# Kernel tuning notes

Hardware: AMD Instinct MI355X
Metric: run time of the kernel (lower is better)

Reference implementation:

```python
import jax, jax.numpy as jnp
import numpy as np

NLAYERS, NHEAD, ATTN_LEN, DMODEL, DHID, NTOKEN = 9, 2, 5, 128, 512, 2
HD = DMODEL // NHEAD
B, T, F = 4, 4096, 128
INV_SQRT_HD = 1.0 / float(np.sqrt(HD))


def setup_inputs() -> dict:
    key = jax.random.key(0)
    ks = iter(jax.random.split(key, 64))
    def w(shape, s=0.02):
        return jax.random.normal(next(ks), shape, jnp.float32) * s
    return dict(
        x=jax.random.normal(next(ks), (B, T, F), jnp.float32),
        conv1_w=w((32, 1, 5, 3)), conv1_b=jnp.zeros((32,), jnp.float32),
        conv2_w=w((64, 32, 1, 12)), conv2_b=jnp.zeros((64,), jnp.float32),
        conv3_w=w((DMODEL, 64, 3, 6)), conv3_b=jnp.zeros((DMODEL,), jnp.float32),
        ln1_s=jnp.ones((NLAYERS, DMODEL), jnp.float32), ln1_b=jnp.zeros((NLAYERS, DMODEL), jnp.float32),
        ln2_s=jnp.ones((NLAYERS, DMODEL), jnp.float32), ln2_b=jnp.zeros((NLAYERS, DMODEL), jnp.float32),
        Wq=w((NLAYERS, DMODEL, DMODEL)), bq=jnp.zeros((NLAYERS, DMODEL), jnp.float32),
        Wk=w((NLAYERS, DMODEL, DMODEL)), bk=jnp.zeros((NLAYERS, DMODEL), jnp.float32),
        Wv=w((NLAYERS, DMODEL, DMODEL)), bv=jnp.zeros((NLAYERS, DMODEL), jnp.float32),
        Wo=w((NLAYERS, DMODEL, DMODEL)), bo=jnp.zeros((NLAYERS, DMODEL), jnp.float32),
        Er=w((NLAYERS, NHEAD, ATTN_LEN, HD)),
        W1=w((NLAYERS, DMODEL, DHID)), b1=jnp.zeros((NLAYERS, DHID), jnp.float32),
        W2=w((NLAYERS, DHID, DMODEL)), b2=jnp.zeros((NLAYERS, DMODEL), jnp.float32),
        Wout=w((DMODEL, NTOKEN)), bout=jnp.zeros((NTOKEN,), jnp.float32),
        Wt=w((DMODEL, 300)), bt=jnp.zeros((300,), jnp.float32),
    )


def _ln(x, s, b, eps=1e-5):
    m = x.mean(-1, keepdims=True)
    v = ((x - m) ** 2).mean(-1, keepdims=True)
    return (x - m) * jax.lax.rsqrt(v + eps) * s + b


def _conv(x, w, b, pad_h):
    y = jax.lax.conv_general_dilated(x, w, (1, 1), ((pad_h, pad_h), (0, 0)),
                                     dimension_numbers=('NCHW', 'OIHW', 'NCHW'))
    return y + b[None, :, None, None]


def _pool3(x):
    # MaxPool2d(kernel=(1,3), stride=(1,3)) on freq axis
    return jax.lax.reduce_window(x, -jnp.inf, jax.lax.max, (1, 1, 1, 3), (1, 1, 1, 3), 'VALID')


def _attn(x, Wq, bq, Wk, bk, Wv, bv, Wo, bo, Er, layer):
    # Dilated windowed attention: query t attends to t + (k - attn_len//2)*2^layer
    Bb, Tt, D = x.shape
    dil = 2 ** layer
    c = ATTN_LEN // 2
    q = (x @ Wq + bq).reshape(Bb, Tt, NHEAD, HD)
    k = (x @ Wk + bk).reshape(Bb, Tt, NHEAD, HD)
    v = (x @ Wv + bv).reshape(Bb, Tt, NHEAD, HD)
    offs = (jnp.arange(Tt)[:, None] + (jnp.arange(ATTN_LEN) - c)[None, :] * dil)  # (T, a)
    valid = (offs >= 0) & (offs < Tt)
    idx = jnp.clip(offs, 0, Tt - 1)
    kg = k[:, idx]  # (B, T, a, H, hd)
    vg = v[:, idx]
    scores = (jnp.einsum('bthd,btahd->bhta', q, kg)
              + jnp.einsum('bthd,had->bhta', q, Er)) * INV_SQRT_HD
    scores = jnp.where(valid[None, None], scores, -jnp.inf)
    a = jax.nn.softmax(scores, axis=-1)
    out = jnp.einsum('bhta,btahd->bthd', a, vg).reshape(Bb, Tt, D)
    return out @ Wo + bo


def _forward(x, conv1_w, conv1_b, conv2_w, conv2_b, conv3_w, conv3_b,
             ln1_s, ln1_b, ln2_s, ln2_b, Wq, bq, Wk, bk, Wv, bv, Wo, bo, Er,
             W1, b1, W2, b2, Wout, bout, Wt, bt):
    h = x[:, None]                                    # (B,1,T,F)
    h = jax.nn.relu(_pool3(_conv(h, conv1_w, conv1_b, 2)))
    h = jax.nn.relu(_pool3(_conv(h, conv2_w, conv2_b, 0)))
    h = jax.nn.relu(_pool3(_conv(h, conv3_w, conv3_b, 1)))  # (B,D,T,1)
    h = h[:, :, :, 0].transpose(0, 2, 1)              # (B,T,D)
    skips = []
    for l in range(NLAYERS):
        skip = _attn(_ln(h, ln1_s[l], ln1_b[l]), Wq[l], bq[l], Wk[l], bk[l],
                     Wv[l], bv[l], Wo[l], bo[l], Er[l], l)
        h = h + skip
        z = _ln(h, ln2_s[l], ln2_b[l])
        h = h + jax.nn.relu(z @ W1[l] + b1[l]) @ W2[l] + b2[l]
        skips.append(skip)
    out = jax.nn.relu(h) @ Wout + bout                # (B,T,ntoken)
    t = jax.nn.relu(sum(skips)).mean(axis=1) @ Wt + bt  # (B,300)
    return out, t


def reference(x, conv1_w, conv1_b, conv2_w, conv2_b, conv3_w, conv3_b,
              ln1_s, ln1_b, ln2_s, ln2_b, Wq, bq, Wk, bk, Wv, bv, Wo, bo, Er,
              W1, b1, W2, b2, Wout, bout, Wt, bt):
    return _forward(x, conv1_w, conv1_b, conv2_w, conv2_b, conv3_w, conv3_b,
                    ln1_s, ln1_b, ln2_s, ln2_b, Wq, bq, Wk, bk, Wv, bv, Wo, bo, Er,
                    W1, b1, W2, b2, Wout, bout, Wt, bt)
```

## Files before the change

### kernel.cpp

```cpp
#include <hip/hip_runtime.h>

#define T_ 4096
#define B_ 4

typedef unsigned short u16;
typedef __bf16 bf16x8 __attribute__((ext_vector_type(8)));
typedef float f32x4 __attribute__((ext_vector_type(4)));

__device__ inline void splitbf(float v, u16& h, u16& l) {
  __bf16 hb = (__bf16)v;
  float r = v - (float)hb;
  __bf16 lb = (__bf16)r;
  h = __builtin_bit_cast(u16, hb);
  l = __builtin_bit_cast(u16, lb);
}

#define MFMA(a,b,c) __builtin_amdgcn_mfma_f32_16x16x32_bf16((a),(b),(c),0,0,0)

__global__ __launch_bounds__(256) void k_conv12m(
    const float* __restrict__ x, const float* __restrict__ w1,
    const float* __restrict__ b1,
    const u16* __restrict__ wh, const u16* __restrict__ wl,
    const float* __restrict__ b2,
    u16* __restrict__ oh, u16* __restrict__ ol)
{
  __shared__ float sx[12][130];
  __shared__ float w1s[480];
  __shared__ float b1s[32];
  __shared__ u16 sh[8*43*40];
  __shared__ u16 sl[8*43*40];
  __shared__ float dmp[4][15][66];
  const int tid = threadIdx.x;
  const int t0 = blockIdx.x * 8;
  const int b = blockIdx.y;
  const float* xb = x + (size_t)b*T_*128;
  for (int i = tid; i < 1536; i += 256) {
    int r = i >> 7, c = i & 127;
    int t = t0 - 2 + r;
    sx[r][c] = (t >= 0 && t < T_) ? xb[t*128 + c] : 0.f;
  }
  for (int i = tid; i < 480; i += 256) w1s[i] = w1[i];
  if (tid < 32) b1s[tid] = b1[tid];
  for (int i = tid; i < 320; i += 256) {
    int tt = i / 40, c = i - tt*40;
    sh[(tt*43 + 42)*40 + c] = 0;
    sl[(tt*43 + 42)*40 + c] = 0;
  }
  __syncthreads();
  {
    const int c1 = tid & 31, tt = tid >> 5;
    float w1r[15];
    #pragma unroll
    for (int i = 0; i < 15; i++) w1r[i] = w1s[c1*15 + i];
    float bb1 = b1s[c1];
    for (int wp = 0; wp < 42; wp++) {
      int c0 = wp*3;
      float s0 = 0.f, s1 = 0.f, s2 = 0.f;
      #pragma unroll
      for (int kh = 0; kh < 5; kh++) {
        float x0 = sx[tt+kh][c0],   x1 = sx[tt+kh][c0+1];
        float x2 = sx[tt+kh][c0+2], x3 = sx[tt+kh][c0+3];
        float x4 = sx[tt+kh][c0+4];
        float wA = w1r[kh*3], wB = w1r[kh*3+1], wC = w1r[kh*3+2];
        s0 += x0*wA + x1*wB + x2*wC;
        s1 += x1*wA + x2*wB + x3*wC;
        s2 += x2*wA + x3*wB + x4*wC;
      }
      float v = fmaxf(fmaxf(fmaxf(s0, s1), s2) + bb1, 0.f);
      u16 hh, ll; splitbf(v, hh, ll);
      int dd = (tt*43 + wp)*40 + c1;
      sh[dd] = hh; sl[dd] = ll;
    }
  }
  __syncthreads();
  const int lane = tid & 63;
  const int wid = tid >> 6;
  const int lr = lane & 15;
  const int lk8 = (lane >> 4) * 8;
  f32x4 acc[2][2][4] = {};
  #pragma unroll 3
  for (int kw = 0; kw < 12; kw++) {
    bf16x8 bh[4], bl[4];
    #pragma unroll
    for (int nf = 0; nf < 4; nf++) {
      int go = ((nf*12 + kw) << 9) + (lane << 3);
      bh[nf] = *(const bf16x8*)(wh + go);
      bl[nf] = *(const bf16x8*)(wl + go);
    }
    #pragma unroll
    for (int tp = 0; tp < 2; tp++) {
      int tloc = wid*2 + tp;
      #pragma unroll
      for (int mf = 0; mf < 2; mf++) {
        int lofs = (tloc*43 + mf*16 + lr + kw)*40 + lk8;
        bf16x8 ah = *(const bf16x8*)&sh[lofs];
        bf16x8 al = *(const bf16x8*)&sl[lofs];
        #pragma unroll
        for (int nf = 0; nf < 4; nf++) {
          acc[tp][mf][nf] = MFMA(ah, bl[nf], acc[tp][mf][nf]);
          acc[tp][mf][nf] = MFMA(al, bh[nf], acc[tp][mf][nf]);
          acc[tp][mf][nf] = MFMA(ah, bh[nf], acc[tp][mf][nf]);
        }
      }
    }
  }
  const int lg = lane >> 4;
  for (int tp = 0; tp < 2; tp++) {
    int t = t0 + wid*2 + tp;
    for (int half = 0; half < 2; half++) {
      #pragma unroll
      for (int mf = 0; mf < 2; mf++)
        #pragma unroll
        for (int r = 0; r < 4; r++) {
          int grow = mf*16 + lg*4 + r;
          int lrow = grow - half*15;
          if (lrow >= 0 && lrow < 15) {
            #pragma unroll
            for (int nf = 0; nf < 4; nf++)
              dmp[wid][lrow][nf*16 + lr] = acc[tp][mf][nf][r];
          }
        }
      asm volatile("s_waitcnt lgkmcnt(0)" ::: "memory");
      #pragma unroll
      for (int it = 0; it < 5; it++) {
        float v = fmaxf(fmaxf(dmp[wid][it*3][lane], dmp[wid][it*3+1][lane]),
                        dmp[wid][it*3+2][lane]);
        v = fmaxf(v + b2[lane], 0.f);
        u16 hh, ll; splitbf(v, hh, ll);
        size_t o = (size_t)((b*T_ + t)*10 + half*5 + it)*64 + lane;
        oh[o] = hh; ol[o] = ll;
      }
      asm volatile("s_waitcnt lgkmcnt(0)" ::: "memory");
    }
  }
}

__global__ __launch_bounds__(256) void k_conv3m(
    const u16* __restrict__ ih, const u16* __restrict__ il,
    const u16* __restrict__ wh, const u16* __restrict__ wl,
    const float* __restrict__ b3, float* __restrict__ hout)
{
  __shared__ u16 sh[18*720];
  __shared__ u16 sl[18*720];
  __shared__ float dmp[48][132];
  const int tid = threadIdx.x;
  const int t0 = (blockIdx.x & 255) * 16;
  const int b = blockIdx.y;
  for (int i = tid; i < 1440; i += 256) {
    int cg = i & 7;
    int w = (i >> 3) % 10;
    int tt = i / 80;
    int t = t0 - 1 + tt;
    int dd = tt*720 + w*72 + cg*8;
    if (t >= 0 && t < T_) {
      size_t so = (size_t)((b*T_ + t)*10 + w)*64 + cg*8;
      *(ulonglong2*)&sh[dd] = *(const ulonglong2*)&ih[so];
      *(ulonglong2*)&sl[dd] = *(const ulonglong2*)&il[so];
    } else {
      ulonglong2 z; z.x = 0; z.y = 0;
      *(ulonglong2*)&sh[dd] = z;
      *(ulonglong2*)&sl[dd] = z;
    }
  }
  __syncthreads();
  const int lane = tid & 63;
  const int wid = tid >> 6;
  const int lr = lane & 15;
  const int lk8 = (lane >> 4) * 8;
  int tlm[3], wom[3];
  #pragma unroll
  for (int mf = 0; mf < 3; mf++) {
    int r = mf*16 + lr;
    tlm[mf] = r / 3;
    wom[mf] = r - tlm[mf]*3;
  }
  f32x4 acc[3][2] = {};
  #pragma unroll 2
  for (int kh = 0; kh < 3; kh++) {
    #pragma unroll
    for (int kw = 0; kw < 6; kw++) {
      #pragma unroll
      for (int chh = 0; chh < 2; chh++) {
        int s = (kh*6 + kw)*2 + chh;
        int ch = chh*32;
        bf16x8 bh[2], bl[2];
        #pragma unroll
        for (int nfl = 0; nfl < 2; nfl++) {
          int go = (((wid*2 + nfl)*36 + s) << 9) + (lane << 3);
          bh[nfl] = *(const bf16x8*)(wh + go);
          bl[nfl] = *(const bf16x8*)(wl + go);
        }
        #pragma unroll
        for (int mf = 0; mf < 3; mf++) {
          int lofs = (tlm[mf] + kh)*720 + (wom[mf] + kw)*72 + ch + lk8;
          bf16x8 ah = *(const bf16x8*)&sh[lofs];
          bf16x8 al = *(const bf16x8*)&sl[lofs];
          #pragma unroll
          for (int nfl = 0; nfl < 2; nfl++) {
            acc[mf][nfl] = MFMA(ah, bl[nfl], acc[mf][nfl]);
            acc[mf][nfl] = MFMA(al, bh[nfl], acc[mf][nfl]);
            acc[mf][nfl] = MFMA(ah, bh[nfl], acc[mf][nfl]);
          }
        }
      }
    }
  }
  const int lg = lane >> 4;
  #pragma unroll
  for (int mf = 0; mf < 3; mf++)
    #pragma unroll
    for (int r = 0; r < 4; r++) {
      int row = mf*16 + lg*4 + r;
      #pragma unroll
      for (int nfl = 0; nfl < 2; nfl++)
        dmp[row][wid*32 + nfl*16 + lr] = acc[mf][nfl][r];
    }
  __syncthreads();
  for (int i = tid; i < 2048; i += 256) {
    int c3 = i & 127;
    int tt = i >> 7;
    float v = fmaxf(fmaxf(dmp[tt*3][c3], dmp[tt*3+1][c3]), dmp[tt*3+2][c3]);
    v = fmaxf(v + b3[c3], 0.f);
    hout[(size_t)(b*T_ + t0 + tt)*128 + c3] = v;
  }
}

__device__ inline float wave_sum(float v) {
  #pragma unroll
  for (int m = 1; m < 64; m <<= 1) v += __shfl_xor(v, m, 64);
  return v;
}

__global__ __launch_bounds__(256) void k_ln(
    const float* __restrict__ in, const float* __restrict__ sc,
    const float* __restrict__ bi, u16* __restrict__ oh, u16* __restrict__ ol)
{
  const int lane = threadIdx.x & 63;
  const int row = blockIdx.x*4 + (threadIdx.x >> 6);
  float a = in[row*128 + lane];
  float c = in[row*128 + 64 + lane];
  float mean = wave_sum(a + c) * (1.f/128.f);
  float d0 = a - mean, d1 = c - mean;
  float var = wave_sum(d0*d0 + d1*d1) * (1.f/128.f);
  float rs = rsqrtf(var + 1e-5f);
  float v0 = d0*rs*sc[lane]    + bi[lane];
  float v1 = d1*rs*sc[64+lane] + bi[64+lane];
  u16 h0, l0, h1, l1;
  splitbf(v0, h0, l0); splitbf(v1, h1, l1);
  oh[row*128 + lane] = h0;      ol[row*128 + lane] = l0;
  oh[row*128 + 64 + lane] = h1; ol[row*128 + 64 + lane] = l1;
}

__device__ inline void prep_fr(const float* __restrict__ src,
                               u16* __restrict__ dh, u16* __restrict__ dl,
                               int K, int N, int matStride, int idx)
{
  int mat = idx / (K*N);
  int rem = idx - mat*(K*N);
  int k = rem / N;
  int n = rem - k*N;
  float v = src[idx];
  u16 h, l; splitbf(v, h, l);
  int nt = n >> 4, ks = k >> 5, ksub = k & 31;
  size_t o = (size_t)mat*matStride + (size_t)((nt*(K>>5) + ks) << 9)
           + (((ksub >> 3) << 4) + (n & 15))*8 + (ksub & 7);
  dh[o] = h; dl[o] = l;
}

__global__ __launch_bounds__(256) void k_wprep_all(
    const float* __restrict__ Wq, const float* __restrict__ Wk,
    const float* __restrict__ Wv, const float* __restrict__ Wo,
    const float* __restrict__ W1, const float* __restrict__ W2,
    const float* __restrict__ c2w, const float* __restrict__ c3w,
    u16* wqkv_h, u16* wqkv_l, u16* wo_h, u16* wo_l,
    u16* w1t_h, u16* w1t_l, u16* w2t_h, u16* w2t_l,
    u16* wc2_h, u16* wc2_l, u16* wc3_h, u16* wc3_l)
{
  const int bid = blockIdx.x;
  const int tid = threadIdx.x;
  if (bid < 576) {
    prep_fr(Wq, wqkv_h, wqkv_l, 128, 128, 49152, bid*256 + tid);
  } else if (bid < 1152) {
    prep_fr(Wk, wqkv_h + 16384, wqkv_l + 16384, 128, 128, 49152, (bid-576)*256 + tid);
  } else if (bid < 1728) {
    prep_fr(Wv, wqkv_h + 32768, wqkv_l + 32768, 128, 128, 49152, (bid-1152)*256 + tid);
  } else if (bid < 2304) {
    prep_fr(Wo, wo_h, wo_l, 128, 128, 16384, (bid-1728)*256 + tid);
  } else if (bid < 4608) {
    prep_fr(W1, w1t_h, w1t_l, 128, 512, 65536, (bid-2304)*256 + tid);
  } else if (bid < 6912) {
    prep_fr(W2, w2t_h, w2t_l, 512, 128, 65536, (bid-4608)*256 + tid);
  } else if (bid < 7008) {
    int idx = (bid-6912)*256 + tid;
    int c2 = idx / 384;
    int rem = idx - c2*384;
    int c1 = rem / 12;
    int kw = rem - c1*12;
    float v = c2w[idx];
    u16 h, l; splitbf(v, h, l);
    size_t o = (size_t)((((c2 >> 4)*12 + kw) << 9))
             + (((c1 >> 3) << 4) + (c2 & 15))*8 + (c1 & 7);
    wc2_h[o] = h; wc2_l[o] = l;
  } else {
    int idx = (bid-7008)*256 + tid;
    int c3 = idx / 1152;
    int rem = idx - c3*1152;
    int c2 = rem / 18;
    int khkw = rem - c2*18;
    float v = c3w[idx];
    u16 h, l; splitbf(v, h, l);
    int s = khkw*2 + (c2 >> 5);
    int c = c2 & 31;
    size_t o = (size_t)((((c3 >> 4)*36 + s) << 9))
             + (((c >> 3) << 4) + (c3 & 15))*8 + (c & 7);
    wc3_h[o] = h; wc3_l[o] = l;
  }
}

__global__ __launch_bounds__(256) void k_gqkv(
    const u16* __restrict__ Ah, const u16* __restrict__ Al,
    const u16* __restrict__ Wh, const u16* __restrict__ Wl,
    const float* __restrict__ bq, const float* __restrict__ bk,
    const float* __restrict__ bv, float* __restrict__ outbase)
{
  __shared__ u16 sAh[16*136], sAl[16*136];
  const int tid = threadIdx.x;
  const int m0 = blockIdx.x * 16;
  const int z = blockIdx.y;
  const u16* wh = Wh + z*16384;
  const u16* wl = Wl + z*16384;
  const float* bias = (z == 0) ? bq : (z == 1) ? bk : bv;
  float* C = outbase + (size_t)z*2097152;
  {
    int row = tid >> 4, c8 = tid & 15;
    *(ulonglong2*)&sAh[row*136 + c8*8] = *(const ulonglong2*)&Ah[(size_t)(m0+row)*128 + c8*8];
    *(ulonglong2*)&sAl[row*136 + c8*8] = *(const ulonglong2*)&Al[(size_t)(m0+row)*128 + c8*8];
  }
  __syncthreads();
  const int lane = tid & 63, nq = tid >> 6;
  const int lr = lane & 15, lg = lane >> 4, l8 = lg*8;
  f32x4 acc[2] = {};
  #pragma unroll
  for (int ks = 0; ks < 4; ks++) {
    bf16x8 ah = *(const bf16x8*)&sAh[lr*136 + ks*32 + l8];
    bf16x8 al = *(const bf16x8*)&sAl[lr*136 + ks*32 + l8];
    #pragma unroll
    for (int nf = 0; nf < 2; nf++) {
      int go = (((nq*2 + nf)*4 + ks) << 9) + (lane << 3);
      bf16x8 bh = *(const bf16x8*)(wh + go);
      bf16x8 bl = *(const bf16x8*)(wl + go);
      acc[nf] = MFMA(ah, bl, acc[nf]);
      acc[nf] = MFMA(al, bh, acc[nf]);
      acc[nf] = MFMA(ah, bh, acc[nf]);
    }
  }
  #pragma unroll
  for (int nf = 0; nf < 2; nf++) {
    int col = nq*32 + nf*16 + lr;
    float bb = bias[col];
    #pragma unroll
    for (int r = 0; r < 4; r++)
      C[(size_t)(m0 + lg*4 + r)*128 + col] = acc[nf][r] + bb;
  }
}

__global__ __launch_bounds__(512) void k_layer(
    const float* __restrict__ qin,
    const float* __restrict__ Er,
    const u16* __restrict__ Woh, const u16* __restrict__ Wol,
    const float* __restrict__ bo,
    const float* __restrict__ sc2, const float* __restrict__ bi2,
    const u16* __restrict__ W1h, const u16* __restrict__ W1l,
    const float* __restrict__ b1,
    const u16* __restrict__ W2h, const u16* __restrict__ W2l,
    const float* __restrict__ b2,
    float* __restrict__ hbuf, float* __restrict__ ssum, int skip_init,
    int do_qkv,
    const float* __restrict__ sc1, const float* __restrict__ bi1,
    const u16* __restrict__ Qh, const u16* __restrict__ Ql,
    const float* __restrict__ bq, const float* __restrict__ bk,
    const float* __restrict__ bv, float* __restrict__ qout, int dil)
{
  __shared__ u16 sAh[32*136], sAl[32*136];
  __shared__ u16 hidH[2][32*136], hidL[2][32*136];
  __shared__ float dmp[32*132];
  const int tid = threadIdx.x, lane = tid & 63, wv = tid >> 6;
  const int m0 = blockIdx.x * 32;
  const int b = m0 >> 12;
  const int t0 = m0 & 4095;
  const float* qb = qin;
  const float* kb = qin + 2097152;
  const float* vb = qin + 4194304;
  for (int rr = 0; rr < 4; rr++) {
    int r = wv*4 + rr;
    int t = t0 + r;
    int bt = m0 + r;
    #pragma unroll
    for (int h = 0; h < 2; h++) {
      float qd = qb[(size_t)bt*128 + h*64 + lane];
      float s[5];
      int tpc_arr[5];
      #pragma unroll
      for (int a = 0; a < 5; a++) {
        int tp = t + (a-2)*dil;
        bool valid = (tp >= 0 && tp < T_);
        int tpc = tp < 0 ? 0 : (tp > T_-1 ? T_-1 : tp);
        tpc_arr[a] = tpc;
        float kd = kb[(size_t)(b*T_ + tpc)*128 + h*64 + lane];
        float er = Er[(h*5 + a)*64 + lane];
        float p = qd * (kd + er);
        p = wave_sum(p);
        s[a] = valid ? p * 0.125f : -1e30f;
      }
      float mx = s[0];
      #pragma unroll
      for (int a = 1; a < 5; a++) mx = fmaxf(mx, s[a]);
      float p[5], psum = 0.f;
      #pragma unroll
      for (int a = 0; a < 5; a++) { p[a] = __expf(s[a]-mx); psum += p[a]; }
      float inv = 1.f/psum;
      float o = 0.f;
      #pragma unroll
      for (int a = 0; a < 5; a++)
        o += p[a] * vb[(size_t)(b*T_ + tpc_arr[a])*128 + h*64 + lane];
      float vo = o * inv;
      u16 hh, ll; splitbf(vo, hh, ll);
      sAh[r*136 + h*64 + lane] = hh;
      sAl[r*136 + h*64 + lane] = ll;
    }
  }
  __syncthreads();
  const int lr = lane & 15, lg = lane >> 4, l8 = lg*8;
  const int mq = wv >> 2, nq = wv & 3;
  {
    f32x4 acc[2] = {};
    #pragma unroll
    for (int ks = 0; ks < 4; ks++) {
      bf16x8 ah = *(const bf16x8*)&sAh[(mq*16 + lr)*136 + ks*32 + l8];
      bf16x8 al = *(const bf16x8*)&sAl[(mq*16 + lr)*136 + ks*32 + l8];
      #pragma unroll
      for (int nf = 0; nf < 2; nf++) {
        int go = (((nq*2 + nf)*4 + ks) << 9) + (lane << 3);
        bf16x8 bh = *(const bf16x8*)(Woh + go);
        bf16x8 bl = *(const bf16x8*)(Wol + go);
        acc[nf] = MFMA(ah, bl, acc[nf]);
        acc[nf] = MFMA(al, bh, acc[nf]);
        acc[nf] = MFMA(ah, bh, acc[nf]);
      }
    }
    #pragma unroll
    for (int nf = 0; nf < 2; nf++) {
      int col = nq*32 + nf*16 + lr;
      float bb = bo[col];
      #pragma unroll
      for (int r = 0; r < 4; r++) {
        int row = mq*16 + lg*4 + r;
        size_t o = (size_t)(m0 + row)*128 + col;
        float val = acc[nf][r] + bb;
        if (skip_init) ssum[o] = val; else ssum[o] += val;
        float hn = hbuf[o] + val;
        hbuf[o] = hn;
        dmp[row*132 + col] = hn;
      }
    }
  }
  __syncthreads();
  {
    const int row = tid >> 4, p = tid & 15;
    float xv[8], s = 0.f;
    const float* dp = &dmp[row*132 + p*8];
    #pragma unroll
    for (int i = 0; i < 8; i++) { xv[i] = dp[i]; s += xv[i]; }
    s += __shfl_xor(s, 1); s += __shfl_xor(s, 2);
    s += __shfl_xor(s, 4); s += __shfl_xor(s, 8);
    float mean = s * (1.f/128.f);
    float v = 0.f;
    #pragma unroll
    for (int i = 0; i < 8; i++) { float d = xv[i]-mean; v += d*d; }
    v += __shfl_xor(v, 1); v += __shfl_xor(v, 2);
    v += __shfl_xor(v, 4); v += __shfl_xor(v, 8);
    float rs = rsqrtf(v*(1.f/128.f) + 1e-5f);
    #pragma unroll
    for (int i = 0; i < 8; i++) {
      int cc = p*8 + i;
      float y = (xv[i]-mean)*rs*sc2[cc] + bi2[cc];
      u16 hh, ll; splitbf(y, hh, ll);
      sAh[row*136 + cc] = hh; sAl[row*136 + cc] = ll;
    }
  }
  __syncthreads();
  f32x4 acc2[2] = {};
  for (int c = 0; c < 4; c++) {
    f32x4 acc1[2] = {};
    #pragma unroll
    for (int ks = 0; ks < 4; ks++) {
      bf16x8 ah = *(const bf16x8*)&sAh[(mq*16 + lr)*136 + ks*32 + l8];
      bf16x8 al = *(const bf16x8*)&sAl[(mq*16 + lr)*136 + ks*32 + l8];
      #pragma unroll
      for (int nf = 0; nf < 2; nf++) {
        int go = (((c*8 + nq*2 + nf)*4 + ks) << 9) + (lane << 3);
        bf16x8 bh = *(const bf16x8*)(W1h + go);
        bf16x8 bl = *(const bf16x8*)(W1l + go);
        acc1[nf] = MFMA(ah, bl, acc1[nf]);
        acc1[nf] = MFMA(al, bh, acc1[nf]);
        acc1[nf] = MFMA(ah, bh, acc1[nf]);
      }
    }
    __syncthreads();
    #pragma unroll
    for (int nf = 0; nf < 2; nf++) {
      int col = nq*32 + nf*16 + lr;
      float bb = b1[c*128 + col];
      #pragma unroll
      for (int r = 0; r < 4; r++) {
        int row = mq*16 + lg*4 + r;
        float hv = fmaxf(acc1[nf][r] + bb, 0.f);
        u16 hh, ll; splitbf(hv, hh, ll);
        hidH[c & 1][row*136 + col] = hh;
        hidL[c & 1][row*136 + col] = ll;
      }
    }
    __syncthreads();
    #pragma unroll
    for (int ks = 0; ks < 4; ks++) {
      bf16x8 ah = *(const bf16x8*)&hidH[c & 1][(mq*16 + lr)*136 + ks*32 + l8];
      bf16x8 al = *(const bf16x8*)&hidL[c & 1][(mq*16 + lr)*136 + ks*32 + l8];
      #pragma unroll
      for (int nf = 0; nf < 2; nf++) {
        int go = (((nq*2 + nf)*16 + c*4 + ks) << 9) + (lane << 3);
        bf16x8 bh = *(const bf16x8*)(W2h + go);
        bf16x8 bl = *(const bf16x8*)(W2l + go);
        acc2[nf] = MFMA(ah, bl, acc2[nf]);
        acc2[nf] = MFMA(al, bh, acc2[nf]);
        acc2[nf] = MFMA(ah, bh, acc2[nf]);
      }
    }
  }
  #pragma unroll
  for (int nf = 0; nf < 2; nf++) {
    int col = nq*32 + nf*16 + lr;
    float bb = b2[col];
    #pragma unroll
    for (int r = 0; r < 4; r++) {
      int row = mq*16 + lg*4 + r;
      size_t o = (size_t)(m0 + row)*128 + col;
      float hn = hbuf[o] + acc2[nf][r] + bb;
      hbuf[o] = hn;
      dmp[row*132 + col] = hn;
    }
  }
  if (!do_qkv) return;
  __syncthreads();
  {
    const int row = tid >> 4, p = tid & 15;
    float xv[8], s = 0.f;
    const float* dp = &dmp[row*132 + p*8];
    #pragma unroll
    for (int i = 0; i < 8; i++) { xv[i] = dp[i]; s += xv[i]; }
    s += __shfl_xor(s, 1); s += __shfl_xor(s, 2);
    s += __shfl_xor(s, 4); s += __shfl_xor(s, 8);
    float mean = s * (1.f/128.f);
    float v = 0.f;
    #pragma unroll
    for (int i = 0; i < 8; i++) { float d = xv[i]-mean; v += d*d; }
    v += __shfl_xor(v, 1); v += __shfl_xor(v, 2);
    v += __shfl_xor(v, 4); v += __shfl_xor(v, 8);
    float rs = rsqrtf(v*(1.f/128.f) + 1e-5f);
    #pragma unroll
    for (int i = 0; i < 8; i++) {
      int cc = p*8 + i;
      float y = (xv[i]-mean)*rs*sc1[cc] + bi1[cc];
      u16 hh, ll; splitbf(y, hh, ll);
      sAh[row*136 + cc] = hh; sAl[row*136 + cc] = ll;
    }
  }
  __syncthreads();
  for (int z = 0; z < 3; z++) {
    const u16* wh = Qh + z*16384;
    const u16* wl = Ql + z*16384;
    const float* bias = (z == 0) ? bq : (z == 1) ? bk : bv;
    float* C = qout + (size_t)z*2097152;
    f32x4 acc[2] = {};
    #pragma unroll
    for (int ks = 0; ks < 4; ks++) {
      bf16x8 ah = *(const bf16x8*)&sAh[(mq*16 + lr)*136 + ks*32 + l8];
      bf16x8 al = *(const bf16x8*)&sAl[(mq*16 + lr)*136 + ks*32 + l8];
      #pragma unroll
      for (int nf = 0; nf < 2; nf++) {
        int go = (((nq*2 + nf)*4 + ks) << 9) + (lane << 3);
        bf16x8 bh = *(const bf16x8*)(wh + go);
        bf16x8 bl = *(const bf16x8*)(wl + go);
        acc[nf] = MFMA(ah, bl, acc[nf]);
        acc[nf] = MFMA(al, bh, acc[nf]);
        acc[nf] = MFMA(ah, bh, acc[nf]);
      }
    }
    #pragma unroll
    for (int nf = 0; nf < 2; nf++) {
      int col = nq*32 + nf*16 + lr;
      float bb = bias[col];
      #pragma unroll
      for (int r = 0; r < 4; r++)
        C[(size_t)(m0 + mq*16 + lg*4 + r)*128 + col] = acc[nf][r] + bb;
    }
  }
}

__global__ __launch_bounds__(256) void k_out(
    const float* __restrict__ h, const float* __restrict__ Wout,
    const float* __restrict__ bout, float* __restrict__ out)
{
  int idx = blockIdx.x*256 + threadIdx.x;
  int bt = idx >> 1, j = idx & 1;
  float acc = bout[j];
  const float* hp = &h[bt*128];
  #pragma unroll 4
  for (int k2 = 0; k2 < 128; k2++)
    acc += fmaxf(hp[k2], 0.f) * Wout[k2*2 + j];
  out[idx] = acc;
}

__global__ __launch_bounds__(256) void k_red1(
    const float* __restrict__ ss, float* __restrict__ part)
{
  __shared__ float red[256];
  int b = blockIdx.x >> 5, g = blockIdx.x & 31;
  int c = threadIdx.x & 127, hf = threadIdx.x >> 7;
  float acc = 0.f;
  for (int i2 = 0; i2 < 64; i2++) {
    int t = g*128 + i2*2 + hf;
    acc += fmaxf(ss[(b*T_ + t)*128 + c], 0.f);
  }
  red[threadIdx.x] = acc;
  __syncthreads();
  if (threadIdx.x < 128)
    part[(b*32+g)*128 + threadIdx.x] = red[threadIdx.x] + red[threadIdx.x+128];
}

__global__ __launch_bounds__(512) void k_tail2(
    const float* __restrict__ part, const float* __restrict__ Wt,
    const float* __restrict__ btb, float* __restrict__ out)
{
  __shared__ float mb[512];
  const int tid = threadIdx.x;
  int b = tid >> 7, c = tid & 127;
  float s = 0.f;
  for (int g = 0; g < 32; g++) s += part[(b*32+g)*128 + c];
  mb[tid] = s * (1.f/4096.f);
  __syncthreads();
  for (int i = tid; i < 1200; i += 512) {
    int bb = i / 300, j = i - bb*300;
    float acc = btb[j];
    #pragma unroll 4
    for (int k2 = 0; k2 < 128; k2++)
      acc += mb[bb*128 + k2] * Wt[k2*300 + j];
    out[32768 + i] = acc;
  }
}

extern "C" void kernel_launch(void* const* d_in, const int* in_sizes, int n_in,
                              void* d_out, int out_size, void* d_ws, size_t ws_size,
                              hipStream_t stream)
{
  const float* x    = (const float*)d_in[0];
  const float* c1w  = (const float*)d_in[1];
  const float* c1b  = (const float*)d_in[2];
  const float* c2w  = (const float*)d_in[3];
  const float* c2b  = (const float*)d_in[4];
  const float* c3w  = (const float*)d_in[5];
  const float* c3b  = (const float*)d_in[6];
  const float* ln1s = (const float*)d_in[7];
  const float* ln1b = (const float*)d_in[8];
  const float* ln2s = (const float*)d_in[9];
  const float* ln2b = (const float*)d_in[10];
  const float* Wq   = (const float*)d_in[11];
  const float* bq   = (const float*)d_in[12];
  const float* Wk   = (const float*)d_in[13];
  const float* bk   = (const float*)d_in[14];
  const float* Wv   = (const float*)d_in[15];
  const float* bv   = (const float*)d_in[16];
  const float* Wo   = (const float*)d_in[17];
  const float* bo   = (const float*)d_in[18];
  const float* Er   = (const float*)d_in[19];
  const float* W1   = (const float*)d_in[20];
  const float* b1   = (const float*)d_in[21];
  const float* W2   = (const float*)d_in[22];
  const float* b2   = (const float*)d_in[23];
  const float* Wout = (const float*)d_in[24];
  const float* bout = (const float*)d_in[25];
  const float* Wt   = (const float*)d_in[26];
  const float* bt   = (const float*)d_in[27];

  char* W = (char*)d_ws;
  u16* c2o_h = (u16*)W;
  u16* c2o_l = (u16*)(W + 20971520);
  char* RB = W + 41943040;
  float* qbuf0 = (float*)RB;
  float* qbuf1 = (float*)(RB + 25165824);
  u16* xh    = (u16*)(RB + 50331648);
  u16* xlo   = (u16*)(RB + 54525952);
  char* RC = W + 100663296;
  float* hbuf = (float*)RC;
  float* ssum = (float*)(RC + 8388608);
  u16* wqkv_h = (u16*)(RC + 16777216);
  u16* wqkv_l = wqkv_h + 442368;
  u16* wo_h   = wqkv_l + 442368;
  u16* wo_l   = wo_h + 147456;
  u16* w1t_h  = wo_l + 147456;
  u16* w1t_l  = w1t_h + 589824;
  u16* w2t_h  = w1t_l + 589824;
  u16* w2t_h2 = w2t_h;  (void)w2t_h2;
  u16* w2t_l  = w2t_h + 589824;
  u16* wc2_h  = w2t_l + 589824;
  u16* wc2_l  = wc2_h + 24576;
  u16* wc3_h  = wc2_l + 24576;
  u16* wc3_l  = wc3_h + 147456;
  float* part  = (float*)(wc3_l + 147456);
  float* outf  = (float*)d_out;

  k_wprep_all<<<7584, 256, 0, stream>>>(
      Wq, Wk, Wv, Wo, W1, W2, c2w, c3w,
      wqkv_h, wqkv_l, wo_h, wo_l, w1t_h, w1t_l, w2t_h, w2t_l,
      wc2_h, wc2_l, wc3_h, wc3_l);

  k_conv12m<<<dim3(512, B_), 256, 0, stream>>>(x, c1w, c1b, wc2_h, wc2_l, c2b,
                                               c2o_h, c2o_l);
  k_conv3m<<<dim3(256, B_), 256, 0, stream>>>(c2o_h, c2o_l, wc3_h, wc3_l, c3b, hbuf);

  k_ln<<<4096, 256, 0, stream>>>(hbuf, ln1s, ln1b, xh, xlo);
  k_gqkv<<<dim3(1024, 3), 256, 0, stream>>>(
      xh, xlo, wqkv_h, wqkv_l, bq, bk, bv, qbuf0);

  for (int l = 0; l < 9; l++) {
    int ln = (l < 8) ? (l + 1) : 0;
    float* qin  = (l & 1) ? qbuf1 : qbuf0;
    float* qout = (l & 1) ? qbuf0 : qbuf1;
    k_layer<<<512, 512, 0, stream>>>(
        qin, Er + l*640,
        wo_h + l*16384, wo_l + l*16384, bo + l*128,
        ln2s + l*128, ln2b + l*128,
        w1t_h + l*65536, w1t_l + l*65536, b1 + l*512,
        w2t_h + l*65536, w2t_l + l*65536, b2 + l*128,
        hbuf, ssum, (l == 0) ? 1 : 0,
        (l < 8) ? 1 : 0,
        ln1s + ln*128, ln1b + ln*128,
        wqkv_h + ln*49152, wqkv_l + ln*49152,
        bq + ln*128, bk + ln*128, bv + ln*128, qout, 1 << l);
  }

  k_out<<<128, 256, 0, stream>>>(hbuf, Wout, bout, outf);
  k_red1<<<128, 256, 0, stream>>>(ssum, part);
  k_tail2<<<1, 512, 0, stream>>>(part, Wt, bt, outf);
}
```

Measured before the change: 671.5 us.

## Fuse LN+QKV prologue, fold output head and skip reduction into last layer

The separate LayerNorm and QKV GEMM kernels are merged into one k_pre0 kernel, so the bf16 hi/lo activation round-trip through global memory goes away. The final layer now computes the output projection and the per-block relu-skip partial sums directly, which removes the k_out and k_red1 launches. k_conv12m is halved per block (4 time steps, twice the blocks) to raise occupancy. k_layer's hidden double buffer is collapsed and aliased with dmp in a union region to cut LDS use, at the cost of an extra barrier.

```diff
diff --git a/kernel.cpp b/kernel.cpp
--- a/kernel.cpp
+++ b/kernel.cpp
@@ -24,36 +24,36 @@
     const float* __restrict__ b2,
     u16* __restrict__ oh, u16* __restrict__ ol)
 {
-  __shared__ float sx[12][130];
+  __shared__ float sx[8][130];
   __shared__ float w1s[480];
   __shared__ float b1s[32];
-  __shared__ u16 sh[8*43*40];
-  __shared__ u16 sl[8*43*40];
+  __shared__ u16 sh[4*43*40];
+  __shared__ u16 sl[4*43*40];
   __shared__ float dmp[4][15][66];
   const int tid = threadIdx.x;
-  const int t0 = blockIdx.x * 8;
+  const int t0 = blockIdx.x * 4;
   const int b = blockIdx.y;
   const float* xb = x + (size_t)b*T_*128;
-  for (int i = tid; i < 1536; i += 256) {
+  for (int i = tid; i < 1024; i += 256) {
     int r = i >> 7, c = i & 127;
     int t = t0 - 2 + r;
     sx[r][c] = (t >= 0 && t < T_) ? xb[t*128 + c] : 0.f;
   }
   for (int i = tid; i < 480; i += 256) w1s[i] = w1[i];
   if (tid < 32) b1s[tid] = b1[tid];
-  for (int i = tid; i < 320; i += 256) {
+  for (int i = tid; i < 160; i += 256) {
     int tt = i / 40, c = i - tt*40;
     sh[(tt*43 + 42)*40 + c] = 0;
     sl[(tt*43 + 42)*40 + c] = 0;
   }
   __syncthreads();
   {
-    const int c1 = tid & 31, tt = tid >> 5;
+    const int c1 = tid & 31, tt = (tid >> 5) & 3, hf = tid >> 7;
     float w1r[15];
     #pragma unroll
     for (int i = 0; i < 15; i++) w1r[i] = w1s[c1*15 + i];
     float bb1 = b1s[c1];
-    for (int wp = 0; wp < 42; wp++) {
+    for (int wp = hf*21; wp < hf*21 + 21; wp++) {
       int c0 = wp*3;
       float s0 = 0.f, s1 = 0.f, s2 = 0.f;
       #pragma unroll
@@ -77,7 +77,7 @@
   const int wid = tid >> 6;
   const int lr = lane & 15;
   const int lk8 = (lane >> 4) * 8;
-  f32x4 acc[2][2][4] = {};
+  f32x4 acc[2][4] = {};
   #pragma unroll 3
   for (int kw = 0; kw < 12; kw++) {
     bf16x8 bh[4], bl[4];
@@ -88,25 +88,21 @@
       bl[nf] = *(const bf16x8*)(wl + go);
     }
     #pragma unroll
-    for (int tp = 0; tp < 2; tp++) {
-      int tloc = wid*2 + tp;
-      #pragma unroll
-      for (int mf = 0; mf < 2; mf++) {
-        int lofs = (tloc*43 + mf*16 + lr + kw)*40 + lk8;
-        bf16x8 ah = *(const bf16x8*)&sh[lofs];
-        bf16x8 al = *(const bf16x8*)&sl[lofs];
-        #pragma unroll
-        for (int nf = 0; nf < 4; nf++) {
-          acc[tp][mf][nf] = MFMA(ah, bl[nf], acc[tp][mf][nf]);
-          acc[tp][mf][nf] = MFMA(al, bh[nf], acc[tp][mf][nf]);
-          acc[tp][mf][nf] = MFMA(ah, bh[nf], acc[tp][mf][nf]);
-        }
+    for (int mf = 0; mf < 2; mf++) {
+      int lofs = (wid*43 + mf*16 + lr + kw)*40 + lk8;
+      bf16x8 ah = *(const bf16x8*)&sh[lofs];
+      bf16x8 al = *(const bf16x8*)&sl[lofs];
+      #pragma unroll
+      for (int nf = 0; nf < 4; nf++) {
+        acc[mf][nf] = MFMA(ah, bl[nf], acc[mf][nf]);
+        acc[mf][nf] = MFMA(al, bh[nf], acc[mf][nf]);
+        acc[mf][nf] = MFMA(ah, bh[nf], acc[mf][nf]);
       }
     }
   }
   const int lg = lane >> 4;
-  for (int tp = 0; tp < 2; tp++) {
-    int t = t0 + wid*2 + tp;
+  {
+    int t = t0 + wid;
     for (int half = 0; half < 2; half++) {
       #pragma unroll
       for (int mf = 0; mf < 2; mf++)
@@ -117,7 +113,7 @@
           if (lrow >= 0 && lrow < 15) {
             #pragma unroll
             for (int nf = 0; nf < 4; nf++)
-              dmp[wid][lrow][nf*16 + lr] = acc[tp][mf][nf][r];
+              dmp[wid][lrow][nf*16 + lr] = acc[mf][nf][r];
           }
         }
       asm volatile("s_waitcnt lgkmcnt(0)" ::: "memory");
@@ -229,26 +225,6 @@
   #pragma unroll
   for (int m = 1; m < 64; m <<= 1) v += __shfl_xor(v, m, 64);
   return v;
-}
-
-__global__ __launch_bounds__(256) void k_ln(
-    const float* __restrict__ in, const float* __restrict__ sc,
-    const float* __restrict__ bi, u16* __restrict__ oh, u16* __restrict__ ol)
-{
-  const int lane = threadIdx.x & 63;
-  const int row = blockIdx.x*4 + (threadIdx.x >> 6);
-  float a = in[row*128 + lane];
-  float c = in[row*128 + 64 + lane];
-  float mean = wave_sum(a + c) * (1.f/128.f);
-  float d0 = a - mean, d1 = c - mean;
-  float var = wave_sum(d0*d0 + d1*d1) * (1.f/128.f);
-  float rs = rsqrtf(var + 1e-5f);
-  float v0 = d0*rs*sc[lane]    + bi[lane];
-  float v1 = d1*rs*sc[64+lane] + bi[64+lane];
-  u16 h0, l0, h1, l1;
-  splitbf(v0, h0, l0); splitbf(v1, h1, l1);
-  oh[row*128 + lane] = h0;      ol[row*128 + lane] = l0;
-  oh[row*128 + 64 + lane] = h1; ol[row*128 + 64 + lane] = l1;
 }
 
 __device__ inline void prep_fr(const float* __restrict__ src,
@@ -317,50 +293,70 @@
   }
 }
 
-__global__ __launch_bounds__(256) void k_gqkv(
-    const u16* __restrict__ Ah, const u16* __restrict__ Al,
-    const u16* __restrict__ Wh, const u16* __restrict__ Wl,
+__global__ __launch_bounds__(512) void k_pre0(
+    const float* __restrict__ hbuf,
+    const float* __restrict__ sc, const float* __restrict__ bi,
+    const u16* __restrict__ Qh, const u16* __restrict__ Ql,
     const float* __restrict__ bq, const float* __restrict__ bk,
-    const float* __restrict__ bv, float* __restrict__ outbase)
+    const float* __restrict__ bv, float* __restrict__ qout)
 {
-  __shared__ u16 sAh[16*136], sAl[16*136];
-  const int tid = threadIdx.x;
-  const int m0 = blockIdx.x * 16;
-  const int z = blockIdx.y;
-  const u16* wh = Wh + z*16384;
-  const u16* wl = Wl + z*16384;
-  const float* bias = (z == 0) ? bq : (z == 1) ? bk : bv;
-  float* C = outbase + (size_t)z*2097152;
+  __shared__ u16 sAh[32*136], sAl[32*136];
+  const int tid = threadIdx.x, lane = tid & 63;
+  const int m0 = blockIdx.x * 32;
   {
-    int row = tid >> 4, c8 = tid & 15;
-    *(ulonglong2*)&sAh[row*136 + c8*8] = *(const ulonglong2*)&Ah[(size_t)(m0+row)*128 + c8*8];
-    *(ulonglong2*)&sAl[row*136 + c8*8] = *(const ulonglong2*)&Al[(size_t)(m0+row)*128 + c8*8];
-  }
-  __syncthreads();
-  const int lane = tid & 63, nq = tid >> 6;
+    const int row = tid >> 4, p = tid & 15;
+    float xv[8], s = 0.f;
+    const float* hp = &hbuf[(size_t)(m0 + row)*128 + p*8];
+    #pragma unroll
+    for (int i = 0; i < 8; i++) { xv[i] = hp[i]; s += xv[i]; }
+    s += __shfl_xor(s, 1); s += __shfl_xor(s, 2);
+    s += __shfl_xor(s, 4); s += __shfl_xor(s, 8);
+    float mean = s * (1.f/128.f);
+    float v = 0.f;
+    #pragma unroll
+    for (int i = 0; i < 8; i++) { float d = xv[i]-mean; v += d*d; }
+    v += __shfl_xor(v, 1); v += __shfl_xor(v, 2);
+    v += __shfl_xor(v, 4); v += __shfl_xor(v, 8);
+    float rs = rsqrtf(v*(1.f/128.f) + 1e-5f);
+    #pragma unroll
+    for (int i = 0; i < 8; i++) {
+      int cc = p*8 + i;
+      float y = (xv[i]-mean)*rs*sc[cc] + bi[cc];
+      u16 hh, ll; splitbf(y, hh, ll);
+      sAh[row*136 + cc] = hh; sAl[row*136 + cc] = ll;
+    }
+  }
+  __syncthreads();
+  const int wv = tid >> 6, mq = wv >> 2, nq = wv & 3;
   const int lr = lane & 15, lg = lane >> 4, l8 = lg*8;
-  f32x4 acc[2] = {};
-  #pragma unroll
-  for (int ks = 0; ks < 4; ks++) {
-    bf16x8 ah = *(const bf16x8*)&sAh[lr*136 + ks*32 + l8];
-    bf16x8 al = *(const bf16x8*)&sAl[lr*136 + ks*32 + l8];
+  for (int z = 0; z < 3; z++) {
+    const u16* wh = Qh + z*16384;
+    const u16* wl = Ql + z*16384;
+    const float* bias = (z == 0) ? bq : (z == 1) ? bk : bv;
+    float* C = qout + (size_t)z*2097152;
+    f32x4 acc[2] = {};
+    #pragma unroll
+    for (int ks = 0; ks < 4; ks++) {
+      bf16x8 ah = *(const bf16x8*)&sAh[(mq*16 + lr)*136 + ks*32 + l8];
+      bf16x8 al = *(const bf16x8*)&sAl[(mq*16 + lr)*136 + ks*32 + l8];
+      #pragma unroll
+      for (int nf = 0; nf < 2; nf++) {
+        int go = (((nq*2 + nf)*4 + ks) << 9) + (lane << 3);
+        bf16x8 bh = *(const bf16x8*)(wh + go);
+        bf16x8 bl = *(const bf16x8*)(wl + go);
+        acc[nf] = MFMA(ah, bl, acc[nf]);
+        acc[nf] = MFMA(al, bh, acc[nf]);
+        acc[nf] = MFMA(ah, bh, acc[nf]);
+      }
+    }
     #pragma unroll
     for (int nf = 0; nf < 2; nf++) {
-      int go = (((nq*2 + nf)*4 + ks) << 9) + (lane << 3);
-      bf16x8 bh = *(const bf16x8*)(wh + go);
-      bf16x8 bl = *(const bf16x8*)(wl + go);
-      acc[nf] = MFMA(ah, bl, acc[nf]);
-      acc[nf] = MFMA(al, bh, acc[nf]);
-      acc[nf] = MFMA(ah, bh, acc[nf]);
-    }
-  }
-  #pragma unroll
-  for (int nf = 0; nf < 2; nf++) {
-    int col = nq*32 + nf*16 + lr;
-    float bb = bias[col];
-    #pragma unroll
-    for (int r = 0; r < 4; r++)
-      C[(size_t)(m0 + lg*4 + r)*128 + col] = acc[nf][r] + bb;
+      int col = nq*32 + nf*16 + lr;
+      float bb = bias[col];
+      #pragma unroll
+      for (int r = 0; r < 4; r++)
+        C[(size_t)(m0 + mq*16 + lg*4 + r)*128 + col] = acc[nf][r] + bb;
+    }
   }
 }
 
@@ -379,11 +375,15 @@
     const float* __restrict__ sc1, const float* __restrict__ bi1,
     const u16* __restrict__ Qh, const u16* __restrict__ Ql,
     const float* __restrict__ bq, const float* __restrict__ bk,
-    const float* __restrict__ bv, float* __restrict__ qout, int dil)
+    const float* __restrict__ bv, float* __restrict__ qout, int dil,
+    const float* __restrict__ Wout, const float* __restrict__ bout,
+    float* __restrict__ part, float* __restrict__ outf)
 {
   __shared__ u16 sAh[32*136], sAl[32*136];
-  __shared__ u16 hidH[2][32*136], hidL[2][32*136];
-  __shared__ float dmp[32*132];
+  __shared__ __align__(16) char ureg[17408];
+  u16* hidH = (u16*)ureg;
+  u16* hidL = (u16*)(ureg + 8704);
+  float* dmp = (float*)ureg;
   const int tid = threadIdx.x, lane = tid & 63, wv = tid >> 6;
   const int m0 = blockIdx.x * 32;
   const int b = m0 >> 12;
@@ -516,15 +516,15 @@
         int row = mq*16 + lg*4 + r;
         float hv = fmaxf(acc1[nf][r] + bb, 0.f);
         u16 hh, ll; splitbf(hv, hh, ll);
-        hidH[c & 1][row*136 + col] = hh;
-        hidL[c & 1][row*136 + col] = ll;
+        hidH[row*136 + col] = hh;
+        hidL[row*136 + col] = ll;
       }
     }
     __syncthreads();
     #pragma unroll
     for (int ks = 0; ks < 4; ks++) {
-      bf16x8 ah = *(const bf16x8*)&hidH[c & 1][(mq*16 + lr)*136 + ks*32 + l8];
-      bf16x8 al = *(const bf16x8*)&hidL[c & 1][(mq*16 + lr)*136 + ks*32 + l8];
+      bf16x8 ah = *(const bf16x8*)&hidH[(mq*16 + lr)*136 + ks*32 + l8];
+      bf16x8 al = *(const bf16x8*)&hidL[(mq*16 + lr)*136 + ks*32 + l8];
       #pragma unroll
       for (int nf = 0; nf < 2; nf++) {
         int go = (((nq*2 + nf)*16 + c*4 + ks) << 9) + (lane << 3);
@@ -536,6 +536,7 @@
       }
     }
   }
+  __syncthreads();
   #pragma unroll
   for (int nf = 0; nf < 2; nf++) {
     int col = nq*32 + nf*16 + lr;
@@ -549,92 +550,96 @@
       dmp[row*132 + col] = hn;
     }
   }
-  if (!do_qkv) return;
-  __syncthreads();
-  {
-    const int row = tid >> 4, p = tid & 15;
-    float xv[8], s = 0.f;
-    const float* dp = &dmp[row*132 + p*8];
-    #pragma unroll
-    for (int i = 0; i < 8; i++) { xv[i] = dp[i]; s += xv[i]; }
-    s += __shfl_xor(s, 1); s += __shfl_xor(s, 2);
-    s += __shfl_xor(s, 4); s += __shfl_xor(s, 8);
-    float mean = s * (1.f/128.f);
-    float v = 0.f;
-    #pragma unroll
-    for (int i = 0; i < 8; i++) { float d = xv[i]-mean; v += d*d; }
-    v += __shfl_xor(v, 1); v += __shfl_xor(v, 2);
-    v += __shfl_xor(v, 4); v += __shfl_xor(v, 8);
-    float rs = rsqrtf(v*(1.f/128.f) + 1e-5f);
-    #pragma unroll
-    for (int i = 0; i < 8; i++) {
-      int cc = p*8 + i;
-      float y = (xv[i]-mean)*rs*sc1[cc] + bi1[cc];
-      u16 hh, ll; splitbf(y, hh, ll);
-      sAh[row*136 + cc] = hh; sAl[row*136 + cc] = ll;
-    }
-  }
-  __syncthreads();
-  for (int z = 0; z < 3; z++) {
-    const u16* wh = Qh + z*16384;
-    const u16* wl = Ql + z*16384;
-    const float* bias = (z == 0) ? bq : (z == 1) ? bk : bv;
-    float* C = qout + (size_t)z*2097152;
-    f32x4 acc[2] = {};
-    #pragma unroll
-    for (int ks = 0; ks < 4; ks++) {
-      bf16x8 ah = *(const bf16x8*)&sAh[(mq*16 + lr)*136 + ks*32 + l8];
-      bf16x8 al = *(const bf16x8*)&sAl[(mq*16 + lr)*136 + ks*32 + l8];
+  __syncthreads();
+  if (do_qkv) {
+    {
+      const int row = tid >> 4, p = tid & 15;
+      float xv[8], s = 0.f;
+      const float* dp = &dmp[row*132 + p*8];
+      #pragma unroll
+      for (int i = 0; i < 8; i++) { xv[i] = dp[i]; s += xv[i]; }
+      s += __shfl_xor(s, 1); s += __shfl_xor(s, 2);
+      s += __shfl_xor(s, 4); s += __shfl_xor(s, 8);
+      float mean = s * (1.f/128.f);
+      float v = 0.f;
+      #pragma unroll
+      for (int i = 0; i < 8; i++) { float d = xv[i]-mean; v += d*d; }
+      v += __shfl_xor(v, 1); v += __shfl_xor(v, 2);
+      v += __shfl_xor(v, 4); v += __shfl_xor(v, 8);
+      float rs = rsqrtf(v*(1.f/128.f) + 1e-5f);
+      #pragma unroll
+      for (int i = 0; i < 8; i++) {
+        int cc = p*8 + i;
+        float y = (xv[i]-mean)*rs*sc1[cc] + bi1[cc];
+        u16 hh, ll; splitbf(y, hh, ll);
+        sAh[row*136 + cc] = hh; sAl[row*136 + cc] = ll;
+      }
+    }
+    __syncthreads();
+    for (int z = 0; z < 3; z++) {
+      const u16* wh = Qh + z*16384;
+      const u16* wl = Ql + z*16384;
+      const float* bias = (z == 0) ? bq : (z == 1) ? bk : bv;
+      float* C = qout + (size_t)z*2097152;
+      f32x4 acc[2] = {};
+      #pragma unroll
+      for (int ks = 0; ks < 4; ks++) {
+        bf16x8 ah = *(const bf16x8*)&sAh[(mq*16 + lr)*136 + ks*32 + l8];
+        bf16x8 al = *(const bf16x8*)&sAl[(mq*16 + lr)*136 + ks*32 + l8];
+        #pragma unroll
+        for (int nf = 0; nf < 2; nf++) {
+          int go = (((nq*2 + nf)*4 + ks) << 9) + (lane << 3);
+          bf16x8 bh = *(const bf16x8*)(wh + go);
+          bf16x8 bl = *(const bf16x8*)(wl + go);
+          acc[nf] = MFMA(ah, bl, acc[nf]);
+          acc[nf] = MFMA(al, bh, acc[nf]);
+          acc[nf] = MFMA(ah, bh, acc[nf]);
+        }
+      }
       #pragma unroll
       for (int nf = 0; nf < 2; nf++) {
-        int go = (((nq*2 + nf)*4 + ks) << 9) + (lane << 3);
-        bf16x8 bh = *(const bf16x8*)(wh + go);
-        bf16x8 bl = *(const bf16x8*)(wl + go);
-        acc[nf] = MFMA(ah, bl, acc[nf]);
-        acc[nf] = MFMA(al, bh, acc[nf]);
-        acc[nf] = MFMA(ah, bh, acc[nf]);
-      }
-    }
-    #pragma unroll
-    for (int nf = 0; nf < 2; nf++) {
-      int col = nq*32 + nf*16 + lr;
-      float bb = bias[col];
-      #pragma unroll
-      for (int r = 0; r < 4; r++)
-        C[(size_t)(m0 + mq*16 + lg*4 + r)*128 + col] = acc[nf][r] + bb;
-    }
-  }
-}
-
-__global__ __launch_bounds__(256) void k_out(
-    const float* __restrict__ h, const float* __restrict__ Wout,
-    const float* __restrict__ bout, float* __restrict__ out)
-{
-  int idx = blockIdx.x*256 + threadIdx.x;
-  int bt = idx >> 1, j = idx & 1;
-  float acc = bout[j];
-  const float* hp = &h[bt*128];
-  #pragma unroll 4
-  for (int k2 = 0; k2 < 128; k2++)
-    acc += fmaxf(hp[k2], 0.f) * Wout[k2*2 + j];
-  out[idx] = acc;
-}
-
-__global__ __launch_bounds__(256) void k_red1(
-    const float* __restrict__ ss, float* __restrict__ part)
-{
-  __shared__ float red[256];
-  int b = blockIdx.x >> 5, g = blockIdx.x & 31;
-  int c = threadIdx.x & 127, hf = threadIdx.x >> 7;
-  float acc = 0.f;
-  for (int i2 = 0; i2 < 64; i2++) {
-    int t = g*128 + i2*2 + hf;
-    acc += fmaxf(ss[(b*T_ + t)*128 + c], 0.f);
-  }
-  red[threadIdx.x] = acc;
-  __syncthreads();
-  if (threadIdx.x < 128)
-    part[(b*32+g)*128 + threadIdx.x] = red[threadIdx.x] + red[threadIdx.x+128];
+        int col = nq*32 + nf*16 + lr;
+        float bb = bias[col];
+        #pragma unroll
+        for (int r = 0; r < 4; r++)
+          C[(size_t)(m0 + mq*16 + lg*4 + r)*128 + col] = acc[nf][r] + bb;
+      }
+    }
+  } else {
+    {
+      const int row = tid >> 4, p = tid & 15;
+      float o0 = 0.f, o1 = 0.f;
+      const float* dp = &dmp[row*132 + p*8];
+      #pragma unroll
+      for (int i = 0; i < 8; i++) {
+        float hv = fmaxf(dp[i], 0.f);
+        o0 += hv * Wout[(p*8 + i)*2];
+        o1 += hv * Wout[(p*8 + i)*2 + 1];
+      }
+      o0 += __shfl_xor(o0, 1); o0 += __shfl_xor(o0, 2);
+      o0 += __shfl_xor(o0, 4); o0 += __shfl_xor(o0, 8);
+      o1 += __shfl_xor(o1, 1); o1 += __shfl_xor(o1, 2);
+      o1 += __shfl_xor(o1, 4); o1 += __shfl_xor(o1, 8);
+      if (p == 0) {
+        outf[(size_t)(m0 + row)*2]     = o0 + bout[0];
+        outf[(size_t)(m0 + row)*2 + 1] = o1 + bout[1];
+      }
+    }
+    __syncthreads();
+    {
+      float* pr = dmp;
+      int c = tid & 127, q = tid >> 7;
+      float s = 0.f;
+      #pragma unroll
+      for (int r = 0; r < 8; r++)
+        s += fmaxf(ssum[(size_t)(m0 + q*8 + r)*128 + c], 0.f);
+      pr[q*128 + c] = s;
+      __syncthreads();
+      if (tid < 128)
+        part[(size_t)blockIdx.x*128 + tid] =
+            pr[tid] + pr[128+tid] + pr[256+tid] + pr[384+tid];
+    }
+  }
 }
 
 __global__ __launch_bounds__(512) void k_tail2(
@@ -645,7 +650,8 @@
   const int tid = threadIdx.x;
   int b = tid >> 7, c = tid & 127;
   float s = 0.f;
-  for (int g = 0; g < 32; g++) s += part[(b*32+g)*128 + c];
+  for (int j = 0; j < 128; j++)
+    s += part[(size_t)(b*128 + j)*128 + c];
   mb[tid] = s * (1.f/4096.f);
   __syncthreads();
   for (int i = tid; i < 1200; i += 512) {
@@ -697,8 +703,6 @@
   char* RB = W + 41943040;
   float* qbuf0 = (float*)RB;
   float* qbuf1 = (float*)(RB + 25165824);
-  u16* xh    = (u16*)(RB + 50331648);
-  u16* xlo   = (u16*)(RB + 54525952);
   char* RC = W + 100663296;
   float* hbuf = (float*)RC;
   float* ssum = (float*)(RC + 8388608);
@@ -709,7 +713,6 @@
   u16* w1t_h  = wo_l + 147456;
   u16* w1t_l  = w1t_h + 589824;
   u16* w2t_h  = w1t_l + 589824;
-  u16* w2t_h2 = w2t_h;  (void)w2t_h2;
   u16* w2t_l  = w2t_h + 589824;
   u16* wc2_h  = w2t_l + 589824;
   u16* wc2_l  = wc2_h + 24576;
@@ -723,13 +726,12 @@
       wqkv_h, wqkv_l, wo_h, wo_l, w1t_h, w1t_l, w2t_h, w2t_l,
       wc2_h, wc2_l, wc3_h, wc3_l);
 
-  k_conv12m<<<dim3(512, B_), 256, 0, stream>>>(x, c1w, c1b, wc2_h, wc2_l, c2b,
-                                               c2o_h, c2o_l);
+  k_conv12m<<<dim3(1024, B_), 256, 0, stream>>>(x, c1w, c1b, wc2_h, wc2_l, c2b,
+                                                c2o_h, c2o_l);
   k_conv3m<<<dim3(256, B_), 256, 0, stream>>>(c2o_h, c2o_l, wc3_h, wc3_l, c3b, hbuf);
 
-  k_ln<<<4096, 256, 0, stream>>>(hbuf, ln1s, ln1b, xh, xlo);
-  k_gqkv<<<dim3(1024, 3), 256, 0, stream>>>(
-      xh, xlo, wqkv_h, wqkv_l, bq, bk, bv, qbuf0);
+  k_pre0<<<512, 512, 0, stream>>>(hbuf, ln1s, ln1b,
+                                  wqkv_h, wqkv_l, bq, bk, bv, qbuf0);
 
   for (int l = 0; l < 9; l++) {
     int ln = (l < 8) ? (l + 1) : 0;
@@ -745,10 +747,9 @@
         (l < 8) ? 1 : 0,
         ln1s + ln*128, ln1b + ln*128,
         wqkv_h + ln*49152, wqkv_l + ln*49152,
-        bq + ln*128, bk + ln*128, bv + ln*128, qout, 1 << l);
-  }
-
-  k_out<<<128, 256, 0, stream>>>(hbuf, Wout, bout, outf);
-  k_red1<<<128, 256, 0, stream>>>(ssum, part);
+        bq + ln*128, bk + ln*128, bv + ln*128, qout, 1 << l,
+        Wout, bout, part, outf);
+  }
+
   k_tail2<<<1, 512, 0, stream>>>(part, Wt, bt, outf);
 }
```

Result: no change. 669.4 us (-0.3%).
